# Optimization experiments

Hardware: AMD Instinct MI355X
Metric: run time of the kernel (lower is better)

The kernel has to match this reference:

```python
import jax, jax.numpy as jnp
import numpy as np

H = 150
PASSES = 5
NSETS = 2
N = 50000
E = 400000
G = 64
SLOPE = 0.01  # torch leaky_relu default


def setup_inputs() -> dict:
    key = jax.random.key(0)
    ks = jax.random.split(key, 20)
    def u(k, shape, fan):
        lim = 1.0 / np.sqrt(fan)
        return jax.random.uniform(k, shape, jnp.float32, -lim, lim)
    return {
        "nodes": jax.random.normal(ks[0], (N, H), jnp.float32),
        "problem_type": jax.random.uniform(ks[1], (G, 1), jnp.float32),
        "edge_W": u(ks[2], (NSETS, H, H), H),
        "edge_b": u(ks[3], (NSETS, H), H),
        "gru_w_ih": u(ks[4], (3 * H, H), H),
        "gru_w_hh": u(ks[5], (3 * H, H), H),
        "gru_b_ih": u(ks[6], (3 * H,), H),
        "gru_b_hh": u(ks[7], (3 * H,), H),
        "fc1_w": u(ks[8], (80, 151), 151),
        "fc1_b": u(ks[9], (80,), 151),
        "fc2_w": u(ks[10], (80, 80), 80),
        "fc2_b": u(ks[11], (80,), 80),
        "fcL_w": u(ks[12], (10, 80), 80),
        "fcL_b": u(ks[13], (10,), 80),
        "edges": jax.random.randint(ks[14], (NSETS, E, 2), 0, N),
        "graph_ids": jnp.sort(jax.random.randint(ks[15], (N,), 0, G)),
        "tbptt": 0,
    }


def _gru_cell(x, h, w_ih, w_hh, b_ih, b_hh):
    gi = x @ w_ih.T + b_ih  # [N, 3H]
    gh = h @ w_hh.T + b_hh
    ir, iz, inn = jnp.split(gi, 3, axis=-1)
    hr, hz, hn = jnp.split(gh, 3, axis=-1)
    r = jax.nn.sigmoid(ir + hr)
    z = jax.nn.sigmoid(iz + hz)
    n = jnp.tanh(inn + r * hn)
    return (1.0 - z) * n + z * h


def reference(nodes, problem_type, edge_W, edge_b, gru_w_ih, gru_w_hh,
              gru_b_ih, gru_b_hh, fc1_w, fc1_b, fc2_w, fc2_b, fcL_w, fcL_b,
              edges, graph_ids, tbptt):
    n_sets = edge_W.shape[0]
    n_graphs = problem_type.shape[0]
    for j in range(PASSES):
        incoming = jnp.zeros_like(nodes)
        for k in range(n_sets):
            src = edges[k, :, 1]
            dst = edges[k, :, 0]
            # NOTE: in the source, the first Linear+leaky_relu result is
            # overwritten; the effective edge message is just the second Linear.
            y = nodes[src] @ edge_W[k].T + edge_b[k]  # [E, H]
            incoming = incoming.at[dst].add(y)
        nodes = _gru_cell(incoming, nodes, gru_w_ih, gru_w_hh, gru_b_ih, gru_b_hh)
        if tbptt == 1 and j < PASSES - 2:
            nodes = jax.lax.stop_gradient(nodes)
    g = jax.ops.segment_sum(nodes, graph_ids, num_segments=n_graphs)  # [G, H]
    g = jnp.log(g)
    g = jnp.where(jnp.isnan(g), 0.0, g)
    g = jax.nn.relu(g)
    x = jnp.concatenate([g, problem_type], axis=1)  # [G, 151]
    x = jax.nn.leaky_relu(x @ fc1_w.T + fc1_b, SLOPE)
    x = jax.nn.leaky_relu(x @ fc2_w.T + fc2_b, SLOPE)
    return x @ fcL_w.T + fcL_b  # [G, 10]
```

## Files before the change

kernel.cpp:

```cpp
#include <hip/hip_runtime.h>
#include <stdint.h>

#define NN 50000
#define H 150
#define NE 400000
#define NG 64
#define NPASS 5
#define KB 480
#define VC 640
#define NRB 391

typedef unsigned short u16;
typedef unsigned int u32;
typedef __attribute__((ext_vector_type(8))) short short8;
typedef __attribute__((ext_vector_type(4))) float float4v;
typedef __attribute__((ext_vector_type(4))) u32 uint4v;

__device__ __forceinline__ u16 f2bf_rn(float x) {
  union { float f; u32 u; } v; v.f = x;
  u32 r = v.u + 0x7fffu + ((v.u >> 16) & 1u);
  return (u16)(r >> 16);
}
__device__ __forceinline__ float bf2f(u16 h) {
  union { u32 u; float f; } v; v.u = ((u32)h) << 16;
  return v.f;
}
__device__ __forceinline__ u32 packf(float v) {
  u16 hi = f2bf_rn(v);
  u16 lo = f2bf_rn(v - bf2f(hi));
  return (u32)hi | ((u32)lo << 16);
}
__device__ __forceinline__ float upk(u32 u) {
  union { u32 u; float f; } a, b;
  a.u = u << 16; b.u = u & 0xffff0000u;
  return a.f + b.f;
}
__device__ __forceinline__ void async16(const void* g, void* l) {
  __builtin_amdgcn_global_load_lds(
      (const __attribute__((address_space(1))) unsigned int*)(uintptr_t)g,
      (__attribute__((address_space(3))) unsigned int*)(uint32_t)(uintptr_t)l,
      16, 0, 0);
}

__global__ void hist_kernel(const int* __restrict__ edges, int* __restrict__ cnt) {
  int id = blockIdx.x * 256 + threadIdx.x;
  if (id >= 2 * NE) return;
  int dst = edges[id * 2];
  int set = id / NE;
  atomicAdd(&cnt[dst * 2 + set], 1);
}

__global__ __launch_bounds__(1024) void scan1_kernel(const int* __restrict__ cnt,
                                                     int* __restrict__ rowptr,
                                                     int* __restrict__ bsum, int n) {
  __shared__ int sd[1024];
  int t = threadIdx.x;
  int idx = blockIdx.x * 1024 + t;
  int v = (idx < n) ? cnt[idx] : 0;
  sd[t] = v;
  __syncthreads();
  for (int off = 1; off < 1024; off <<= 1) {
    int add = (t >= off) ? sd[t - off] : 0;
    __syncthreads();
    sd[t] += add;
    __syncthreads();
  }
  if (idx < n) rowptr[idx] = sd[t] - v;
  if (t == 1023) bsum[blockIdx.x] = sd[1023];
}

__global__ __launch_bounds__(128) void scan2_kernel(const int* __restrict__ bsum,
                                                    int* __restrict__ boff, int nb) {
  __shared__ int sd[128];
  int t = threadIdx.x;
  int v = (t < nb) ? bsum[t] : 0;
  sd[t] = v;
  __syncthreads();
  for (int off = 1; off < 128; off <<= 1) {
    int add = (t >= off) ? sd[t - off] : 0;
    __syncthreads();
    sd[t] += add;
    __syncthreads();
  }
  boff[t] = sd[t] - v;
}

__global__ void scan3_kernel(int* __restrict__ rowptr, const int* __restrict__ boff, int n) {
  int idx = blockIdx.x * 256 + threadIdx.x;
  if (idx < n) rowptr[idx] += boff[idx >> 10];
}

__global__ void total_kernel(int* __restrict__ rowptr, const int* __restrict__ boff, int n, int nb) {
  if (threadIdx.x == 0 && blockIdx.x == 0) rowptr[n] = boff[nb];
}

__global__ void copy_int_kernel(const int* __restrict__ a, int* __restrict__ b, int n) {
  int id = blockIdx.x * 256 + threadIdx.x;
  if (id < n) b[id] = a[id];
}

__global__ void fill_kernel(const int* __restrict__ edges, int* __restrict__ cursor,
                            u16* __restrict__ colbuf) {
  int id = blockIdx.x * 256 + threadIdx.x;
  if (id >= 2 * NE) return;
  int dst = edges[id * 2];
  int src = edges[id * 2 + 1];
  int set = id / NE;
  int pos = atomicAdd(&cursor[dst * 2 + set], 1);
  colbuf[pos] = (u16)src;
}

__global__ void bounds_kernel(const int* __restrict__ gids, int* __restrict__ gstart) {
  int g = threadIdx.x;
  if (g > NG) return;
  int lo = 0, hi = NN;
  while (lo < hi) { int m = (lo + hi) >> 1; if (gids[m] < g) lo = m + 1; else hi = m; }
  gstart[g] = lo;
}

__global__ void build_B_kernel(const float* __restrict__ wih, const float* __restrict__ whh,
                               const float* __restrict__ eW,
                               u16* __restrict__ Bh, u16* __restrict__ Bl) {
  int id = blockIdx.x * 256 + threadIdx.x;
  if (id >= VC * KB) return;
  int v = id / KB, k = id % KB;
  int g = (v >> 4) & 3, c = (v >> 6) * 16 + (v & 15);
  int seg = k / 160, kk = k % 160;
  float val = 0.f;
  if (c < H && kk < H) {
    if (seg < 2) {
      if (g < 3) {
        const float* wr = wih + (size_t)(g * H + c) * H;
        const float* wc = eW + (size_t)seg * H * H + kk;
        float acc = 0.f;
        for (int t = 0; t < H; t++) acc += wr[t] * wc[(size_t)t * H];
        val = acc;
      }
    } else {
      if (g == 0) val = whh[(size_t)c * H + kk];
      else if (g == 1) val = whh[(size_t)(H + c) * H + kk];
      else if (g == 3) val = whh[(size_t)(2 * H + c) * H + kk];
    }
  }
  u16 h = f2bf_rn(val);
  Bh[id] = h;
  Bl[id] = f2bf_rn(val - bf2f(h));
}

__global__ void build_coef_kernel(const float* __restrict__ wih,
                                  const float* __restrict__ eb,
                                  const float* __restrict__ bih, const float* __restrict__ bhh,
                                  float* __restrict__ coefs) {
  int id = threadIdx.x + blockIdx.x * 256;
  if (id >= VC) return;
  int g = id / 160, c = id % 160;
  float u0 = 0.f, u1 = 0.f, bs = 0.f;
  if (c < H) {
    if (g < 3) {
      const float* wr = wih + (size_t)(g * H + c) * H;
      for (int t = 0; t < H; t++) { u0 += wr[t] * eb[t]; u1 += wr[t] * eb[H + t]; }
    }
    if (g == 0) bs = bih[c] + bhh[c];
    else if (g == 1) bs = bih[H + c] + bhh[H + c];
    else if (g == 2) bs = bih[2 * H + c];
    else bs = bhh[2 * H + c];
  }
  coefs[id] = u0;
  coefs[VC + id] = u1;
  coefs[2 * VC + id] = bs;
}

__global__ void init_nodes_kernel(const float* __restrict__ nin,
                                  u32* __restrict__ npkA, u32* __restrict__ npkB) {
  int id = blockIdx.x * 256 + threadIdx.x;
  if (id >= NN * 160) return;
  int r = id / 160, c = id % 160;
  if (c < H) {
    npkA[id] = packf(nin[(size_t)r * H + c]);
  } else {
    npkA[id] = 0;
    npkB[id] = 0;
  }
}

__global__ void pad_S_kernel(u16* __restrict__ Sh, u16* __restrict__ Sl) {
  int id = blockIdx.x * 256 + threadIdx.x;
  if (id >= NN * 20) return;
  int r = id / 20, rem = id % 20;
  int set = rem / 10, t = rem % 10;
  size_t off = (size_t)r * 320 + set * 160 + H + t;
  Sh[off] = 0; Sl[off] = 0;
}

__global__ __launch_bounds__(256) void gather_kernel(
    const u32* __restrict__ npk, const int* __restrict__ rowptr,
    const u16* __restrict__ colbuf, u16* __restrict__ Sh, u16* __restrict__ Sl) {
  int gtid = blockIdx.x * 256 + threadIdx.x;
  int node = gtid >> 6;
  int lane = gtid & 63;
  if (node >= NN) return;
  int s = rowptr[2 * node], mid = rowptr[2 * node + 1], e = rowptr[2 * node + 2];
  int c0 = lane, c1 = lane + 64, c2 = lane + 128;
  bool ok2 = (c2 < H);
  float a0 = 0.f, a1 = 0.f, a2 = 0.f;
  int p = s;
  for (; p + 1 < mid; p += 2) {
    const u32* rA = npk + (size_t)colbuf[p] * 160;
    const u32* rB = npk + (size_t)colbuf[p + 1] * 160;
    u32 xa0 = rA[c0], xa1 = rA[c1];
    u32 xb0 = rB[c0], xb1 = rB[c1];
    u32 xa2 = 0, xb2 = 0;
    if (ok2) { xa2 = rA[c2]; xb2 = rB[c2]; }
    a0 += upk(xa0) + upk(xb0);
    a1 += upk(xa1) + upk(xb1);
    if (ok2) a2 += upk(xa2) + upk(xb2);
  }
  if (p < mid) {
    const u32* rA = npk + (size_t)colbuf[p] * 160;
    a0 += upk(rA[c0]); a1 += upk(rA[c1]); if (ok2) a2 += upk(rA[c2]);
  }
  float b0 = 0.f, b1 = 0.f, b2 = 0.f;
  p = mid;
  for (; p + 1 < e; p += 2) {
    const u32* rA = npk + (size_t)colbuf[p] * 160;
    const u32* rB = npk + (size_t)colbuf[p + 1] * 160;
    u32 xa0 = rA[c0], xa1 = rA[c1];
    u32 xb0 = rB[c0], xb1 = rB[c1];
    u32 xa2 = 0, xb2 = 0;
    if (ok2) { xa2 = rA[c2]; xb2 = rB[c2]; }
    b0 += upk(xa0) + upk(xb0);
    b1 += upk(xa1) + upk(xb1);
    if (ok2) b2 += upk(xa2) + upk(xb2);
  }
  if (p < e) {
    const u32* rA = npk + (size_t)colbuf[p] * 160;
    b0 += upk(rA[c0]); b1 += upk(rA[c1]); if (ok2) b2 += upk(rA[c2]);
  }
  u16* oh = Sh + (size_t)node * 320;
  u16* ol = Sl + (size_t)node * 320;
  u16 h;
  h = f2bf_rn(a0); oh[c0] = h; ol[c0] = f2bf_rn(a0 - bf2f(h));
  h = f2bf_rn(a1); oh[c1] = h; ol[c1] = f2bf_rn(a1 - bf2f(h));
  if (ok2) { h = f2bf_rn(a2); oh[c2] = h; ol[c2] = f2bf_rn(a2 - bf2f(h)); }
  h = f2bf_rn(b0); oh[160 + c0] = h; ol[160 + c0] = f2bf_rn(b0 - bf2f(h));
  h = f2bf_rn(b1); oh[160 + c1] = h; ol[160 + c1] = f2bf_rn(b1 - bf2f(h));
  if (ok2) { h = f2bf_rn(b2); oh[160 + c2] = h; ol[160 + c2] = f2bf_rn(b2 - bf2f(h)); }
}

__global__ __launch_bounds__(256) void gru_gemm_kernel(
    const u16* __restrict__ Sh, const u16* __restrict__ Sl,
    const u32* __restrict__ npkc,
    const u16* __restrict__ Bh, const u16* __restrict__ Bl,
    const float* __restrict__ coefs, const int* __restrict__ rowptr,
    u32* __restrict__ npkn) {
  __shared__ char Abuf[16384];
  __shared__ char Bbuf[16384];
  const int bid = blockIdx.x;
  const int xcd = bid & 7;
  const int rest = bid >> 3;
  const int ccb = rest % 5;
  const int r0b = (rest / 5) * 8 + xcd;
  if (r0b >= NRB) return;
  const int r0 = r0b * 128;
  const int tid = threadIdx.x;
  const int w = tid >> 6, l = tid & 63;
  const int m = l & 15, quad = l >> 4;
  const int mrow0 = (w & 1) * 64;
  const int nco0 = (w >> 1) * 64;

  float4v acc[4][4];
  #pragma unroll
  for (int mt = 0; mt < 4; mt++)
    #pragma unroll
    for (int j = 0; j < 4; j++) acc[mt][j] = (float4v){0.f, 0.f, 0.f, 0.f};

  #pragma unroll 1
  for (int kt = 0; kt < 10; kt++) {
    int koff = kt * 32;
    #pragma unroll
    for (int i = 0; i < 2; i++) {
      int cl = i * 256 + tid;
      int row = cl >> 2;
      int q = (cl & 3) ^ ((row >> 1) & 3);
      int rg = min(r0 + row, NN - 1);
      size_t go = (size_t)rg * 320 + koff + q * 8;
      int lb = i * 4096 + w * 1024;
      async16(Sh + go, Abuf + lb);
      async16(Sl + go, Abuf + 8192 + lb);
      size_t gb = (size_t)(ccb * 128 + row) * KB + koff + q * 8;
      async16(Bh + gb, Bbuf + lb);
      async16(Bl + gb, Bbuf + 8192 + lb);
    }
    __syncthreads();
    short8 bh[4], bl[4];
    #pragma unroll
    for (int j = 0; j < 4; j++) {
      int br = nco0 + j * 16 + m;
      int bd = br * 64 + ((quad ^ ((br >> 1) & 3)) * 16);
      bh[j] = *(const short8*)(Bbuf + bd);
      bl[j] = *(const short8*)(Bbuf + 8192 + bd);
    }
    #pragma unroll
    for (int mt = 0; mt < 4; mt++) {
      int r = mrow0 + mt * 16 + m;
      int ad = r * 64 + ((quad ^ ((r >> 1) & 3)) * 16);
      short8 ah = *(const short8*)(Abuf + ad);
      short8 al = *(const short8*)(Abuf + 8192 + ad);
      #pragma unroll
      for (int j = 0; j < 4; j++) {
        acc[mt][j] = __builtin_amdgcn_mfma_f32_16x16x32_bf16(ah, bh[j], acc[mt][j], 0, 0, 0);
        acc[mt][j] = __builtin_amdgcn_mfma_f32_16x16x32_bf16(ah, bl[j], acc[mt][j], 0, 0, 0);
        acc[mt][j] = __builtin_amdgcn_mfma_f32_16x16x32_bf16(al, bh[j], acc[mt][j], 0, 0, 0);
      }
    }
    __syncthreads();
  }

  #pragma unroll 1
  for (int kt = 0; kt < 5; kt++) {
    int koff = kt * 32;
    #pragma unroll
    for (int i = 0; i < 4; i++) {
      int cl = i * 256 + tid;
      int row = cl >> 3;
      int q = (cl & 7) ^ (row & 7);
      int rg = min(r0 + row, NN - 1);
      async16(npkc + (size_t)rg * 160 + koff + q * 4, Abuf + i * 4096 + w * 1024);
    }
    #pragma unroll
    for (int i = 0; i < 2; i++) {
      int cl = i * 256 + tid;
      int row = cl >> 2;
      int q = (cl & 3) ^ ((row >> 1) & 3);
      size_t gb = (size_t)(ccb * 128 + row) * KB + 320 + koff + q * 8;
      int lb = i * 4096 + w * 1024;
      async16(Bh + gb, Bbuf + lb);
      async16(Bl + gb, Bbuf + 8192 + lb);
    }
    __syncthreads();
    short8 bh[4], bl[4];
    #pragma unroll
    for (int j = 0; j < 4; j++) {
      int br = nco0 + j * 16 + m;
      int bd = br * 64 + ((quad ^ ((br >> 1) & 3)) * 16);
      bh[j] = *(const short8*)(Bbuf + bd);
      bl[j] = *(const short8*)(Bbuf + 8192 + bd);
    }
    #pragma unroll
    for (int mt = 0; mt < 4; mt++) {
      int r = mrow0 + mt * 16 + m;
      uint4v p0 = *(const uint4v*)(Abuf + r * 128 + (((2 * quad) ^ (r & 7)) * 16));
      uint4v p1 = *(const uint4v*)(Abuf + r * 128 + (((2 * quad + 1) ^ (r & 7)) * 16));
      u32 uu[8] = {p0.x, p0.y, p0.z, p0.w, p1.x, p1.y, p1.z, p1.w};
      short8 ah, al;
      #pragma unroll
      for (int e2 = 0; e2 < 8; e2++) {
        ah[e2] = (short)(uu[e2] & 0xffffu);
        al[e2] = (short)(uu[e2] >> 16);
      }
      #pragma unroll
      for (int j = 0; j < 4; j++) {
        acc[mt][j] = __builtin_amdgcn_mfma_f32_16x16x32_bf16(ah, bh[j], acc[mt][j], 0, 0, 0);
        acc[mt][j] = __builtin_amdgcn_mfma_f32_16x16x32_bf16(ah, bl[j], acc[mt][j], 0, 0, 0);
        acc[mt][j] = __builtin_amdgcn_mfma_f32_16x16x32_bf16(al, bh[j], acc[mt][j], 0, 0, 0);
      }
    }
    __syncthreads();
  }

  int c = (ccb * 2 + (w >> 1)) * 16 + m;
  if (c >= H) return;
  float u0r = coefs[c],            u0z = coefs[160 + c],
        u0n = coefs[320 + c];
  float u1r = coefs[VC + c],       u1z = coefs[VC + 160 + c],
        u1n = coefs[VC + 320 + c];
  float bsr = coefs[2 * VC + c],   bsz = coefs[2 * VC + 160 + c],
        bsn = coefs[2 * VC + 320 + c], bsh = coefs[2 * VC + 480 + c];
  #pragma unroll
  for (int mt = 0; mt < 4; mt++) {
    #pragma unroll
    for (int i = 0; i < 4; i++) {
      int row = r0 + mrow0 + mt * 16 + quad * 4 + i;
      if (row >= NN) continue;
      float d0 = (float)(rowptr[2 * row + 1] - rowptr[2 * row]);
      float d1 = (float)(rowptr[2 * row + 2] - rowptr[2 * row + 1]);
      float pr = acc[mt][0][i] + d0 * u0r + d1 * u1r + bsr;
      float pz = acc[mt][1][i] + d0 * u0z + d1 * u1z + bsz;
      float pn = acc[mt][2][i] + d0 * u0n + d1 * u1n + bsn;
      float ph = acc[mt][3][i] + bsh;
      float r_g = 1.f / (1.f + __expf(-pr));
      float z_g = 1.f / (1.f + __expf(-pz));
      float narg = pn + r_g * ph;
      float e2 = __expf(2.f * narg);
      float n_g = 1.f - 2.f / (e2 + 1.f);
      float h = upk(npkc[(size_t)row * 160 + c]);
      npkn[(size_t)row * 160 + c] = packf((1.f - z_g) * n_g + z_g * h);
    }
  }
}

__global__ __launch_bounds__(192) void segsum_kernel(const u32* __restrict__ npk,
                                                     const int* __restrict__ gstart,
                                                     float* __restrict__ gsum) {
  int g = blockIdx.x, chunk = blockIdx.y;
  int c = threadIdx.x;
  if (c >= H) return;
  int s = gstart[g], e = gstart[g + 1];
  int len = e - s;
  if (len <= 0) return;
  int per = (len + 3) / 4;
  int rs = s + chunk * per;
  int re = min(e, rs + per);
  if (rs >= re) return;
  float acc = 0.f;
  for (int r = rs; r < re; r++) acc += upk(npk[(size_t)r * 160 + c]);
  atomicAdd(&gsum[g * H + c], acc);
}

__global__ __launch_bounds__(192) void head_kernel(
    const float* __restrict__ gsum, const float* __restrict__ pt,
    const float* __restrict__ fc1_w, const float* __restrict__ fc1_b,
    const float* __restrict__ fc2_w, const float* __restrict__ fc2_b,
    const float* __restrict__ fcL_w, const float* __restrict__ fcL_b,
    float* __restrict__ out) {
  __shared__ float x[151];
  __shared__ float x1[80];
  __shared__ float x2[80];
  int row = blockIdx.x;
  int t = threadIdx.x;
  if (t < 151) {
    float v;
    if (t < H) { float g = gsum[row * H + t]; v = (g > 1.f) ? logf(g) : 0.f; }
    else v = pt[row];
    x[t] = v;
  }
  __syncthreads();
  if (t < 80) {
    float acc = fc1_b[t];
    const float* wrow = fc1_w + t * 151;
    #pragma unroll 4
    for (int k = 0; k < 151; k++) acc += x[k] * wrow[k];
    x1[t] = (acc > 0.f) ? acc : 0.01f * acc;
  }
  __syncthreads();
  if (t < 80) {
    float acc = fc2_b[t];
    const float* wrow = fc2_w + t * 80;
    #pragma unroll 4
    for (int k = 0; k < 80; k++) acc += x1[k] * wrow[k];
    x2[t] = (acc > 0.f) ? acc : 0.01f * acc;
  }
  __syncthreads();
  if (t < 10) {
    float acc = fcL_b[t];
    const float* wrow = fcL_w + t * 80;
    #pragma unroll 4
    for (int k = 0; k < 80; k++) acc += x2[k] * wrow[k];
    out[row * 10 + t] = acc;
  }
}

extern "C" void kernel_launch(void* const* d_in, const int* in_sizes, int n_in,
                              void* d_out, int out_size, void* d_ws, size_t ws_size,
                              hipStream_t stream) {
  const float* nodes_in = (const float*)d_in[0];
  const float* problem_type = (const float*)d_in[1];
  const float* edge_W = (const float*)d_in[2];
  const float* edge_b = (const float*)d_in[3];
  const float* w_ih = (const float*)d_in[4];
  const float* w_hh = (const float*)d_in[5];
  const float* b_ih = (const float*)d_in[6];
  const float* b_hh = (const float*)d_in[7];
  const float* fc1_w = (const float*)d_in[8];
  const float* fc1_b = (const float*)d_in[9];
  const float* fc2_w = (const float*)d_in[10];
  const float* fc2_b = (const float*)d_in[11];
  const float* fcL_w = (const float*)d_in[12];
  const float* fcL_b = (const float*)d_in[13];
  const int* edges = (const int*)d_in[14];
  const int* graph_ids = (const int*)d_in[15];

  char* ws = (char*)d_ws;
  size_t off = 0;
  auto alloc = [&](size_t bytes) -> void* {
    void* p = ws + off;
    off = (off + bytes + 255) & ~(size_t)255;
    return p;
  };
  u32* npkA     = (u32*)alloc((size_t)NN * 160 * 4);
  u32* npkB     = (u32*)alloc((size_t)NN * 160 * 4);
  u16* Sh       = (u16*)alloc((size_t)NN * 320 * 2);
  u16* Sl       = (u16*)alloc((size_t)NN * 320 * 2);
  u16* Bh       = (u16*)alloc((size_t)VC * KB * 2);
  u16* Bl       = (u16*)alloc((size_t)VC * KB * 2);
  float* coefs  = (float*)alloc(3 * VC * 4);
  int* rowptr   = (int*)alloc((2 * NN + 1) * 4);
  int* cursor   = (int*)alloc(2 * NN * 4);
  u16* colbuf   = (u16*)alloc(2ull * NE * 2);
  int* bsum     = (int*)alloc(128 * 4);
  int* boff     = (int*)alloc(128 * 4);
  int* gstart   = (int*)alloc((NG + 1) * 4);
  float* gsum   = (float*)alloc((size_t)NG * H * 4);

  const int n2 = 2 * NN;
  const int nb = (n2 + 1023) / 1024;

  hipMemsetAsync(cursor, 0, n2 * 4, stream);
  hist_kernel<<<(2 * NE + 255) / 256, 256, 0, stream>>>(edges, cursor);
  scan1_kernel<<<nb, 1024, 0, stream>>>(cursor, rowptr, bsum, n2);
  scan2_kernel<<<1, 128, 0, stream>>>(bsum, boff, nb);
  scan3_kernel<<<(n2 + 255) / 256, 256, 0, stream>>>(rowptr, boff, n2);
  total_kernel<<<1, 64, 0, stream>>>(rowptr, boff, n2, nb);
  copy_int_kernel<<<(n2 + 255) / 256, 256, 0, stream>>>(rowptr, cursor, n2);
  fill_kernel<<<(2 * NE + 255) / 256, 256, 0, stream>>>(edges, cursor, colbuf);
  bounds_kernel<<<1, 128, 0, stream>>>(graph_ids, gstart);
  build_B_kernel<<<(VC * KB + 255) / 256, 256, 0, stream>>>(w_ih, w_hh, edge_W, Bh, Bl);
  build_coef_kernel<<<(VC + 255) / 256, 256, 0, stream>>>(w_ih, edge_b, b_ih, b_hh, coefs);
  init_nodes_kernel<<<(NN * 160 + 255) / 256, 256, 0, stream>>>(nodes_in, npkA, npkB);
  pad_S_kernel<<<(NN * 20 + 255) / 256, 256, 0, stream>>>(Sh, Sl);

  const int ngrp = (NRB + 7) / 8;
  u32* nbuf[2] = {npkA, npkB};
  for (int pass = 0; pass < NPASS; pass++) {
    u32* cur = nbuf[pass & 1];
    u32* nxt = nbuf[1 - (pass & 1)];
    gather_kernel<<<(NN * 64 + 255) / 256, 256, 0, stream>>>(cur, rowptr, colbuf, Sh, Sl);
    gru_gemm_kernel<<<ngrp * 5 * 8, 256, 0, stream>>>(
        Sh, Sl, cur, Bh, Bl, coefs, rowptr, nxt);
  }
  u32* fin = nbuf[NPASS & 1];

  hipMemsetAsync(gsum, 0, (size_t)NG * H * 4, stream);
  segsum_kernel<<<dim3(NG, 4), 192, 0, stream>>>(fin, gstart, gsum);
  head_kernel<<<NG, 192, 0, stream>>>(gsum, problem_type, fc1_w, fc1_b, fc2_w, fc2_b,
                                      fcL_w, fcL_b, (float*)d_out);
}
```

Before: 1.284 ms.

## Double-buffer GRU GEMM LDS tiles and skip structurally-zero weight column tiles

Merges the two K-loops into one 15-step loop that prefetches the next K tile into a second LDS buffer while computing the current one. It also skips loading and multiplying one of four 16-column weight tiles per wave in each phase, tiles the packed weight layout leaves unused. This cuts both load latency stalls and MFMA work. LDS use doubles to 64KB per block, which may lower occupancy.

```diff
diff --git a/kernel.cpp b/kernel.cpp
--- a/kernel.cpp
+++ b/kernel.cpp
@@ -253,8 +253,8 @@
     const u16* __restrict__ Bh, const u16* __restrict__ Bl,
     const float* __restrict__ coefs, const int* __restrict__ rowptr,
     u32* __restrict__ npkn) {
-  __shared__ char Abuf[16384];
-  __shared__ char Bbuf[16384];
+  __shared__ char Abuf[2][16384];
+  __shared__ char Bbuf[2][16384];
   const int bid = blockIdx.x;
   const int xcd = bid & 7;
   const int rest = bid >> 3;
@@ -274,97 +274,113 @@
     #pragma unroll
     for (int j = 0; j < 4; j++) acc[mt][j] = (float4v){0.f, 0.f, 0.f, 0.f};
 
+  auto stage = [&](int kt, char* Ab, char* Bb) {
+    if (kt < 10) {
+      int koff = kt * 32;
+      #pragma unroll
+      for (int i = 0; i < 2; i++) {
+        int cl = i * 256 + tid;
+        int row = cl >> 2;
+        int q = (cl & 3) ^ ((row >> 1) & 3);
+        int rg = min(r0 + row, NN - 1);
+        size_t go = (size_t)rg * 320 + koff + q * 8;
+        int lb = i * 4096 + w * 1024;
+        async16(Sh + go, Ab + lb);
+        async16(Sl + go, Ab + 8192 + lb);
+        if (((row >> 4) & 3) != 3) {
+          size_t gb = (size_t)(ccb * 128 + row) * KB + koff + q * 8;
+          async16(Bh + gb, Bb + lb);
+          async16(Bl + gb, Bb + 8192 + lb);
+        }
+      }
+    } else {
+      int koff = (kt - 10) * 32;
+      #pragma unroll
+      for (int i = 0; i < 4; i++) {
+        int cl = i * 256 + tid;
+        int row = cl >> 3;
+        int q = (cl & 7) ^ (row & 7);
+        int rg = min(r0 + row, NN - 1);
+        async16(npkc + (size_t)rg * 160 + koff + q * 4, Ab + i * 4096 + w * 1024);
+      }
+      #pragma unroll
+      for (int i = 0; i < 2; i++) {
+        int cl = i * 256 + tid;
+        int row = cl >> 2;
+        int q = (cl & 3) ^ ((row >> 1) & 3);
+        if (((row >> 4) & 3) != 2) {
+          size_t gb = (size_t)(ccb * 128 + row) * KB + 320 + koff + q * 8;
+          int lb = i * 4096 + w * 1024;
+          async16(Bh + gb, Bb + lb);
+          async16(Bl + gb, Bb + 8192 + lb);
+        }
+      }
+    }
+  };
+
+  auto compute = [&](int kt, const char* Ab, const char* Bb) {
+    if (kt < 10) {
+      short8 bh[3], bl[3];
+      #pragma unroll
+      for (int j = 0; j < 3; j++) {
+        int br = nco0 + j * 16 + m;
+        int bd = br * 64 + ((quad ^ ((br >> 1) & 3)) * 16);
+        bh[j] = *(const short8*)(Bb + bd);
+        bl[j] = *(const short8*)(Bb + 8192 + bd);
+      }
+      #pragma unroll
+      for (int mt = 0; mt < 4; mt++) {
+        int r = mrow0 + mt * 16 + m;
+        int ad = r * 64 + ((quad ^ ((r >> 1) & 3)) * 16);
+        short8 ah = *(const short8*)(Ab + ad);
+        short8 al = *(const short8*)(Ab + 8192 + ad);
+        #pragma unroll
+        for (int j = 0; j < 3; j++) {
+          acc[mt][j] = __builtin_amdgcn_mfma_f32_16x16x32_bf16(ah, bh[j], acc[mt][j], 0, 0, 0);
+          acc[mt][j] = __builtin_amdgcn_mfma_f32_16x16x32_bf16(ah, bl[j], acc[mt][j], 0, 0, 0);
+          acc[mt][j] = __builtin_amdgcn_mfma_f32_16x16x32_bf16(al, bh[j], acc[mt][j], 0, 0, 0);
+        }
+      }
+    } else {
+      const int jmap[3] = {0, 1, 3};
+      short8 bh[3], bl[3];
+      #pragma unroll
+      for (int jj = 0; jj < 3; jj++) {
+        int br = nco0 + jmap[jj] * 16 + m;
+        int bd = br * 64 + ((quad ^ ((br >> 1) & 3)) * 16);
+        bh[jj] = *(const short8*)(Bb + bd);
+        bl[jj] = *(const short8*)(Bb + 8192 + bd);
+      }
+      #pragma unroll
+      for (int mt = 0; mt < 4; mt++) {
+        int r = mrow0 + mt * 16 + m;
+        uint4v p0 = *(const uint4v*)(Ab + r * 128 + (((2 * quad) ^ (r & 7)) * 16));
+        uint4v p1 = *(const uint4v*)(Ab + r * 128 + (((2 * quad + 1) ^ (r & 7)) * 16));
+        u32 uu[8] = {p0.x, p0.y, p0.z, p0.w, p1.x, p1.y, p1.z, p1.w};
+        short8 ah, al;
+        #pragma unroll
+        for (int e2 = 0; e2 < 8; e2++) {
+          ah[e2] = (short)(uu[e2] & 0xffffu);
+          al[e2] = (short)(uu[e2] >> 16);
+        }
+        #pragma unroll
+        for (int jj = 0; jj < 3; jj++) {
+          int j = jmap[jj];
+          acc[mt][j] = __builtin_amdgcn_mfma_f32_16x16x32_bf16(ah, bh[jj], acc[mt][j], 0, 0, 0);
+          acc[mt][j] = __builtin_amdgcn_mfma_f32_16x16x32_bf16(ah, bl[jj], acc[mt][j], 0, 0, 0);
+          acc[mt][j] = __builtin_amdgcn_mfma_f32_16x16x32_bf16(al, bh[jj], acc[mt][j], 0, 0, 0);
+        }
+      }
+    }
+  };
+
+  stage(0, Abuf[0], Bbuf[0]);
+  __syncthreads();
   #pragma unroll 1
-  for (int kt = 0; kt < 10; kt++) {
-    int koff = kt * 32;
-    #pragma unroll
-    for (int i = 0; i < 2; i++) {
-      int cl = i * 256 + tid;
-      int row = cl >> 2;
-      int q = (cl & 3) ^ ((row >> 1) & 3);
-      int rg = min(r0 + row, NN - 1);
-      size_t go = (size_t)rg * 320 + koff + q * 8;
-      int lb = i * 4096 + w * 1024;
-      async16(Sh + go, Abuf + lb);
-      async16(Sl + go, Abuf + 8192 + lb);
-      size_t gb = (size_t)(ccb * 128 + row) * KB + koff + q * 8;
-      async16(Bh + gb, Bbuf + lb);
-      async16(Bl + gb, Bbuf + 8192 + lb);
-    }
-    __syncthreads();
-    short8 bh[4], bl[4];
-    #pragma unroll
-    for (int j = 0; j < 4; j++) {
-      int br = nco0 + j * 16 + m;
-      int bd = br * 64 + ((quad ^ ((br >> 1) & 3)) * 16);
-      bh[j] = *(const short8*)(Bbuf + bd);
-      bl[j] = *(const short8*)(Bbuf + 8192 + bd);
-    }
-    #pragma unroll
-    for (int mt = 0; mt < 4; mt++) {
-      int r = mrow0 + mt * 16 + m;
-      int ad = r * 64 + ((quad ^ ((r >> 1) & 3)) * 16);
-      short8 ah = *(const short8*)(Abuf + ad);
-      short8 al = *(const short8*)(Abuf + 8192 + ad);
-      #pragma unroll
-      for (int j = 0; j < 4; j++) {
-        acc[mt][j] = __builtin_amdgcn_mfma_f32_16x16x32_bf16(ah, bh[j], acc[mt][j], 0, 0, 0);
-        acc[mt][j] = __builtin_amdgcn_mfma_f32_16x16x32_bf16(ah, bl[j], acc[mt][j], 0, 0, 0);
-        acc[mt][j] = __builtin_amdgcn_mfma_f32_16x16x32_bf16(al, bh[j], acc[mt][j], 0, 0, 0);
-      }
-    }
-    __syncthreads();
-  }
-
-  #pragma unroll 1
-  for (int kt = 0; kt < 5; kt++) {
-    int koff = kt * 32;
-    #pragma unroll
-    for (int i = 0; i < 4; i++) {
-      int cl = i * 256 + tid;
-      int row = cl >> 3;
-      int q = (cl & 7) ^ (row & 7);
-      int rg = min(r0 + row, NN - 1);
-      async16(npkc + (size_t)rg * 160 + koff + q * 4, Abuf + i * 4096 + w * 1024);
-    }
-    #pragma unroll
-    for (int i = 0; i < 2; i++) {
-      int cl = i * 256 + tid;
-      int row = cl >> 2;
-      int q = (cl & 3) ^ ((row >> 1) & 3);
-      size_t gb = (size_t)(ccb * 128 + row) * KB + 320 + koff + q * 8;
-      int lb = i * 4096 + w * 1024;
-      async16(Bh + gb, Bbuf + lb);
-      async16(Bl + gb, Bbuf + 8192 + lb);
-    }
-    __syncthreads();
-    short8 bh[4], bl[4];
-    #pragma unroll
-    for (int j = 0; j < 4; j++) {
-      int br = nco0 + j * 16 + m;
-      int bd = br * 64 + ((quad ^ ((br >> 1) & 3)) * 16);
-      bh[j] = *(const short8*)(Bbuf + bd);
-      bl[j] = *(const short8*)(Bbuf + 8192 + bd);
-    }
-    #pragma unroll
-    for (int mt = 0; mt < 4; mt++) {
-      int r = mrow0 + mt * 16 + m;
-      uint4v p0 = *(const uint4v*)(Abuf + r * 128 + (((2 * quad) ^ (r & 7)) * 16));
-      uint4v p1 = *(const uint4v*)(Abuf + r * 128 + (((2 * quad + 1) ^ (r & 7)) * 16));
-      u32 uu[8] = {p0.x, p0.y, p0.z, p0.w, p1.x, p1.y, p1.z, p1.w};
-      short8 ah, al;
-      #pragma unroll
-      for (int e2 = 0; e2 < 8; e2++) {
-        ah[e2] = (short)(uu[e2] & 0xffffu);
-        al[e2] = (short)(uu[e2] >> 16);
-      }
-      #pragma unroll
-      for (int j = 0; j < 4; j++) {
-        acc[mt][j] = __builtin_amdgcn_mfma_f32_16x16x32_bf16(ah, bh[j], acc[mt][j], 0, 0, 0);
-        acc[mt][j] = __builtin_amdgcn_mfma_f32_16x16x32_bf16(ah, bl[j], acc[mt][j], 0, 0, 0);
-        acc[mt][j] = __builtin_amdgcn_mfma_f32_16x16x32_bf16(al, bh[j], acc[mt][j], 0, 0, 0);
-      }
-    }
+  for (int kt = 0; kt < 15; kt++) {
+    int cur = kt & 1;
+    if (kt + 1 < 15) stage(kt + 1, Abuf[cur ^ 1], Bbuf[cur ^ 1]);
+    compute(kt, Abuf[cur], Bbuf[cur]);
     __syncthreads();
   }
 
```

Result: faster. 1.173 ms (-8.6%).
